# Performance work log

Measured on AMD Instinct MI355X. Metric: run time of the kernel, lower is better.

Reference implementation:

```python
import jax, jax.numpy as jnp
import numpy as np

NUM_SPECIES = 7
B, A, F = 1024, 48, 384


def setup_inputs() -> dict:
    key = jax.random.key(0)
    ks = jax.random.split(key, 10)
    species = jax.random.randint(ks[0], (B, A), 0, NUM_SPECIES, dtype=jnp.int32)
    aev = jax.random.normal(ks[1], (B, A, F), dtype=jnp.float32)
    def w(k, shape, fan_in):
        s = 1.0 / np.sqrt(fan_in).astype(np.float32)
        return jax.random.uniform(k, shape, jnp.float32, -s, s)
    return {
        "species": species,
        "aev": aev,
        "W1": w(ks[2], (NUM_SPECIES, 256, 384), 384),
        "b1": w(ks[3], (NUM_SPECIES, 256), 384),
        "W2": w(ks[4], (NUM_SPECIES, 192, 256), 256),
        "b2": w(ks[5], (NUM_SPECIES, 192), 256),
        "W3": w(ks[6], (NUM_SPECIES, 160, 192), 192),
        "b3": w(ks[7], (NUM_SPECIES, 160), 192),
        "W4": w(ks[8], (NUM_SPECIES, 1, 160), 160),
        "b4": w(ks[9], (NUM_SPECIES, 1), 160),
    }


def reference(species, aev, W1, b1, W2, b2, W3, b3, W4, b4):
    # species: [B, A] int, aev: [B, A, 384]
    celu = lambda x: jax.nn.celu(x, alpha=0.1)

    def expert(s):
        # Per-species MLP 384->256->192->160->1 applied to all atoms; selected via mask.
        h = celu(jnp.einsum('baf,hf->bah', aev, W1[s]) + b1[s])
        h = celu(jnp.einsum('bah,gh->bag', h, W2[s]) + b2[s])
        h = celu(jnp.einsum('bag,eg->bae', h, W3[s]) + b3[s])
        return (jnp.einsum('bae,oe->bao', h, W4[s]) + b4[s])[..., 0]  # [B, A]

    atom_energy = jnp.zeros(species.shape, aev.dtype)
    for s in range(NUM_SPECIES):  # fixed small expert loop (hard routing)
        atom_energy = jnp.where(species == s, expert(s), atom_energy)
    # scatter-sum atomic energies into per-molecule energies
    return atom_energy.sum(axis=1)  # [B]
```

## Files before the change

### kernel.cpp

```cpp
#include <hip/hip_runtime.h>
#include <math.h>

#define NSPEC 7
#define NMOL 1024
#define APM 48
#define NATOMS (NMOL * APM)
#define FDIM 384

typedef unsigned short u16;
typedef unsigned int u32;
typedef unsigned long long u64;
typedef __attribute__((ext_vector_type(8))) short short8;
typedef __attribute__((ext_vector_type(4))) float floatx4;

#define W1_ELEMS_PER_S (16 * 12 * 64 * 8)
#define W2_ELEMS_PER_S (12 * 8 * 64 * 8)
#define W3_ELEMS_PER_S (10 * 6 * 64 * 8)

#define BUCKET_BLOCKS (NATOMS / 256)
#define PACK1_BLOCKS (NSPEC * 16)
#define PACK2_BLOCKS (NSPEC * 12)
#define PACK3_BLOCKS (NSPEC * 10)
#define PREP_BLOCKS (BUCKET_BLOCKS + PACK1_BLOCKS + PACK2_BLOCKS + PACK3_BLOCKS)

#define MLP_BLOCKS 3078

#define WS_W1_OFF 32
#define WS_W2_OFF (WS_W1_OFF + 1376256)
#define WS_W3_OFF (WS_W2_OFF + 688128)
#define WS_BKT_OFF (WS_W3_OFF + 430080)

#define BUFST 264

__device__ __forceinline__ float celu01(float x) {
    float e = fmaf(0.1f, __expf(x * 10.0f), -0.1f);
    return x > 0.0f ? x : e;
}

__device__ __forceinline__ u16 bfr(float f) {
    u32 u = __float_as_uint(f);
    u += 0x7fffu + ((u >> 16) & 1u);
    return (u16)(u >> 16);
}

__device__ __forceinline__ float bf2f(short s) {
    return __uint_as_float(((u32)(u16)s) << 16);
}

union U8 { short8 v; u16 u[8]; };
union U4 { u64 ll; u16 u[4]; };

template <int KGS, int NTILES>
__device__ __forceinline__ void pack_tile(const float* __restrict__ W,
                                          u16* __restrict__ dst,
                                          int s, int t2, u16* lds) {
    const int K = KGS * 32;
    const int K4 = K / 4;
    int t = threadIdx.x;
    const float* wbase = W + ((size_t)(s * NTILES + t2) * 16) * K;
    for (int i = t; i < 16 * K4; i += 256) {
        int r = i / K4, c = i % K4;
        float4 v = ((const float4*)(wbase + (size_t)r * K))[c];
        u16* d = lds + r * K + c * 4;
        d[0] = bfr(v.x); d[1] = bfr(v.y); d[2] = bfr(v.z); d[3] = bfr(v.w);
    }
    __syncthreads();
    int w = t >> 6, lane = t & 63;
    int n = lane & 15, ks = lane >> 4;
    for (int kg = w; kg < KGS; kg += 4) {
        short8 v = *reinterpret_cast<const short8*>(lds + n * K + kg * 32 + ks * 8);
        *reinterpret_cast<short8*>(
            dst + (((size_t)(s * NTILES + t2) * KGS + kg) * 64 + lane) * 8) = v;
    }
}

__global__ void prep_kernel(const int* __restrict__ species,
                            int* __restrict__ g_cnt, u16* __restrict__ bucket,
                            const float* __restrict__ W1, const float* __restrict__ W2,
                            const float* __restrict__ W3,
                            u16* __restrict__ w1p, u16* __restrict__ w2p,
                            u16* __restrict__ w3p, float* __restrict__ out) {
    __shared__ u16 lds[16 * 384];
    __shared__ int l_cnt[NSPEC];
    __shared__ int l_base[NSPEC];
    int t = threadIdx.x;
    int bx = blockIdx.x;
    if (bx < BUCKET_BLOCKS) {
        if (bx == 0) {
            float4 z = {0.f, 0.f, 0.f, 0.f};
            ((float4*)out)[t] = z;
        }
        if (t < NSPEC) l_cnt[t] = 0;
        __syncthreads();
        int i = bx * 256 + t;
        int s = species[i];
        int lpos = atomicAdd(&l_cnt[s], 1);
        __syncthreads();
        if (t < NSPEC) l_base[t] = atomicAdd(&g_cnt[t], l_cnt[t]);
        __syncthreads();
        bucket[s * NATOMS + l_base[s] + lpos] = (u16)i;
    } else if (bx < BUCKET_BLOCKS + PACK1_BLOCKS) {
        int pid = bx - BUCKET_BLOCKS;
        pack_tile<12, 16>(W1, w1p, pid / 16, pid % 16, lds);
    } else if (bx < BUCKET_BLOCKS + PACK1_BLOCKS + PACK2_BLOCKS) {
        int pid = bx - (BUCKET_BLOCKS + PACK1_BLOCKS);
        pack_tile<8, 12>(W2, w2p, pid / 12, pid % 12, lds);
    } else {
        int pid = bx - (BUCKET_BLOCKS + PACK1_BLOCKS + PACK2_BLOCKS);
        pack_tile<6, 10>(W3, w3p, pid / 10, pid % 10, lds);
    }
}

template <int KGS, int NT, int DEPTH>
__device__ __forceinline__ void run_layer16(const short8* af,
                                            const u16* __restrict__ wsp,
                                            const float* __restrict__ bias,
                                            u16* __restrict__ outbuf, int lane) {
    const int HALF = KGS / 2;
    const int NH = NT * 2;
    const int nl = lane & 15, kg4 = lane >> 4;
    const u16* wb = wsp + (size_t)lane * 8;
    short8 b[DEPTH][HALF];
#pragma unroll
    for (int p = 0; p < DEPTH - 1; ++p)
#pragma unroll
        for (int k = 0; k < HALF; ++k)
            b[p][k] = *reinterpret_cast<const short8*>(wb + ((size_t)p * HALF + k) * 512);
    floatx4 acc = {0.f, 0.f, 0.f, 0.f};
#pragma unroll
    for (int h = 0; h < NH; ++h) {
        int pre = h + DEPTH - 1;
        if (pre < NH) {
#pragma unroll
            for (int k = 0; k < HALF; ++k)
                b[pre % DEPTH][k] = *reinterpret_cast<const short8*>(wb + ((size_t)pre * HALF + k) * 512);
        }
#pragma unroll
        for (int k = 0; k < HALF; ++k)
            acc = __builtin_amdgcn_mfma_f32_16x16x32_bf16(b[h % DEPTH][k], af[(h & 1) * HALF + k], acc, 0, 0, 0);
        if (h & 1) {
            int t = h >> 1;
            floatx4 bn = *reinterpret_cast<const floatx4*>(bias + t * 16 + kg4 * 4);
            U4 pk;
#pragma unroll
            for (int r = 0; r < 4; ++r)
                pk.u[r] = bfr(celu01(acc[r] + bn[r]));
            *reinterpret_cast<u64*>(outbuf + (size_t)nl * BUFST + t * 16 + kg4 * 4) = pk.ll;
            acc = (floatx4){0.f, 0.f, 0.f, 0.f};
        }
    }
}

template <int KGS>
__device__ __forceinline__ void load_a16(const u16* __restrict__ buf,
                                         short8* af, int lane) {
    int nl = lane & 15, kg4 = lane >> 4;
#pragma unroll
    for (int kg = 0; kg < KGS; ++kg)
        af[kg] = *reinterpret_cast<const short8*>(buf + (size_t)nl * BUFST + kg * 32 + kg4 * 8);
}

__global__ __launch_bounds__(64, 2) void mlp_kernel(
    const float* __restrict__ aev,
    const u16* __restrict__ w1p, const u16* __restrict__ w2p, const u16* __restrict__ w3p,
    const float* __restrict__ b1, const float* __restrict__ b2, const float* __restrict__ b3,
    const float* __restrict__ W4, const float* __restrict__ b4,
    const int* __restrict__ g_cnt, const u16* __restrict__ bucket,
    float* __restrict__ out) {
    int bx = blockIdx.x;
    int s = -1, chunk = 0;
    {
        int acc = 0;
#pragma unroll
        for (int q = 0; q < NSPEC; ++q) {
            int nb = (g_cnt[q] + 15) >> 4;
            if (s < 0 && bx < acc + nb) { s = q; chunk = bx - acc; }
            acc += nb;
        }
        if (s < 0) return;
    }
    int cnt = g_cnt[s];
    int lane = threadIdx.x & 63;
    int base = chunk * 16;

    __shared__ __align__(16) u16 buf[16 * BUFST];

    int nl = lane & 15, kg4 = lane >> 4;

    short8 af[12];
    {
        int i0 = base + nl;  if (i0 >= cnt) i0 = cnt - 1;
        int a0 = (int)bucket[s * NATOMS + i0];
        const float* ar0 = aev + (size_t)a0 * FDIM;
#pragma unroll
        for (int kg = 0; kg < 12; ++kg) {
            const float4* p0 = (const float4*)(ar0 + kg * 32 + kg4 * 8);
            float4 a = p0[0], b = p0[1];
            U8 x;
            x.u[0] = bfr(a.x); x.u[1] = bfr(a.y); x.u[2] = bfr(a.z); x.u[3] = bfr(a.w);
            x.u[4] = bfr(b.x); x.u[5] = bfr(b.y); x.u[6] = bfr(b.z); x.u[7] = bfr(b.w);
            af[kg] = x.v;
        }
    }
    run_layer16<12, 16, 4>(af, w1p + (size_t)s * W1_ELEMS_PER_S, b1 + s * 256, buf, lane);

    short8 c[8];
    load_a16<8>(buf, c, lane);
    run_layer16<8, 12, 4>(c, w2p + (size_t)s * W2_ELEMS_PER_S, b2 + s * 192, buf, lane);

    short8 d[6];
    load_a16<6>(buf, d, lane);
    run_layer16<6, 10, 4>(d, w3p + (size_t)s * W3_ELEMS_PER_S, b3 + s * 160, buf, lane);

    {
        int m = lane >> 2, q = lane & 3;
        const u16* h = buf + (size_t)m * BUFST + q * 40;
        const float* w4s = W4 + s * 160 + q * 40;
        float p = 0.f;
#pragma unroll
        for (int cc = 0; cc < 5; ++cc) {
            short8 hv = *reinterpret_cast<const short8*>(h + cc * 8);
            const float4* wp4 = (const float4*)(w4s + cc * 8);
            float4 wa = wp4[0], wb = wp4[1];
            p += bf2f(hv[0]) * wa.x + bf2f(hv[1]) * wa.y + bf2f(hv[2]) * wa.z + bf2f(hv[3]) * wa.w;
            p += bf2f(hv[4]) * wb.x + bf2f(hv[5]) * wb.y + bf2f(hv[6]) * wb.z + bf2f(hv[7]) * wb.w;
        }
        p += __shfl_down(p, 2, 4);
        p += __shfl_down(p, 1, 4);
        int idx = base + m;
        if (q == 0 && idx < cnt) {
            int atom = (int)bucket[s * NATOMS + idx];
            atomicAdd(&out[atom / APM], p + b4[s]);
        }
    }
}

extern "C" void kernel_launch(void* const* d_in, const int* in_sizes, int n_in,
                              void* d_out, int out_size, void* d_ws, size_t ws_size,
                              hipStream_t stream) {
    const int* species = (const int*)d_in[0];
    const float* aev = (const float*)d_in[1];
    const float* W1 = (const float*)d_in[2];
    const float* b1 = (const float*)d_in[3];
    const float* W2 = (const float*)d_in[4];
    const float* b2 = (const float*)d_in[5];
    const float* W3 = (const float*)d_in[6];
    const float* b3 = (const float*)d_in[7];
    const float* W4 = (const float*)d_in[8];
    const float* b4 = (const float*)d_in[9];
    float* out = (float*)d_out;

    unsigned char* wsb = (unsigned char*)d_ws;
    int* g_cnt = (int*)wsb;
    u16* w1p = (u16*)(wsb + WS_W1_OFF);
    u16* w2p = (u16*)(wsb + WS_W2_OFF);
    u16* w3p = (u16*)(wsb + WS_W3_OFF);
    u16* bucket = (u16*)(wsb + WS_BKT_OFF);

    hipMemsetAsync(g_cnt, 0, 8 * sizeof(int), stream);

    prep_kernel<<<PREP_BLOCKS, 256, 0, stream>>>(
        species, g_cnt, bucket, W1, W2, W3, w1p, w2p, w3p, out);

    mlp_kernel<<<MLP_BLOCKS, 64, 0, stream>>>(
        aev, w1p, w2p, w3p, b1, b2, b3, W4, b4, g_cnt, bucket, out);
}
```

Measured before the change: 180.2 us.

## Share packed weight tiles across four waves via double-buffered LDS staging

Measured after the change: 187.0 us. +3.8%, slower.

```diff
diff --git a/kernel.cpp b/kernel.cpp
--- a/kernel.cpp
+++ b/kernel.cpp
@@ -23,7 +23,7 @@
 #define PACK3_BLOCKS (NSPEC * 10)
 #define PREP_BLOCKS (BUCKET_BLOCKS + PACK1_BLOCKS + PACK2_BLOCKS + PACK3_BLOCKS)
 
-#define MLP_BLOCKS 3078
+#define MLP_BLOCKS 774
 
 #define WS_W1_OFF 32
 #define WS_W2_OFF (WS_W1_OFF + 1376256)
@@ -31,6 +31,12 @@
 #define WS_BKT_OFF (WS_W3_OFF + 430080)
 
 #define BUFST 264
+#define SLOT_U16 6144
+
+#define GLD_LDS(gsrc, ldst)                                                   \
+    __builtin_amdgcn_global_load_lds(                                         \
+        (const __attribute__((address_space(1))) unsigned int*)(gsrc),        \
+        (__attribute__((address_space(3))) unsigned int*)(ldst), 16, 0, 0)
 
 __device__ __forceinline__ float celu01(float x) {
     float e = fmaf(0.1f, __expf(x * 10.0f), -0.1f);
@@ -111,43 +117,42 @@
     }
 }
 
-template <int KGS, int NT, int DEPTH>
-__device__ __forceinline__ void run_layer16(const short8* af,
-                                            const u16* __restrict__ wsp,
-                                            const float* __restrict__ bias,
-                                            u16* __restrict__ outbuf, int lane) {
-    const int HALF = KGS / 2;
-    const int NH = NT * 2;
+template <int KGS, int NT, int SWEEPS>
+__device__ __forceinline__ void run_layer_staged(
+    const short8* af, const u16* __restrict__ wsp,
+    const float* __restrict__ bias,
+    u16* __restrict__ outbuf,
+    u16* __restrict__ sb, int lane, int w) {
     const int nl = lane & 15, kg4 = lane >> 4;
-    const u16* wb = wsp + (size_t)lane * 8;
-    short8 b[DEPTH][HALF];
-#pragma unroll
-    for (int p = 0; p < DEPTH - 1; ++p)
-#pragma unroll
-        for (int k = 0; k < HALF; ++k)
-            b[p][k] = *reinterpret_cast<const short8*>(wb + ((size_t)p * HALF + k) * 512);
-    floatx4 acc = {0.f, 0.f, 0.f, 0.f};
-#pragma unroll
-    for (int h = 0; h < NH; ++h) {
-        int pre = h + DEPTH - 1;
-        if (pre < NH) {
-#pragma unroll
-            for (int k = 0; k < HALF; ++k)
-                b[pre % DEPTH][k] = *reinterpret_cast<const short8*>(wb + ((size_t)pre * HALF + k) * 512);
-        }
-#pragma unroll
-        for (int k = 0; k < HALF; ++k)
-            acc = __builtin_amdgcn_mfma_f32_16x16x32_bf16(b[h % DEPTH][k], af[(h & 1) * HALF + k], acc, 0, 0, 0);
-        if (h & 1) {
-            int t = h >> 1;
-            floatx4 bn = *reinterpret_cast<const floatx4*>(bias + t * 16 + kg4 * 4);
-            U4 pk;
-#pragma unroll
-            for (int r = 0; r < 4; ++r)
-                pk.u[r] = bfr(celu01(acc[r] + bn[r]));
-            *reinterpret_cast<u64*>(outbuf + (size_t)nl * BUFST + t * 16 + kg4 * 4) = pk.ll;
-            acc = (floatx4){0.f, 0.f, 0.f, 0.f};
-        }
+#pragma unroll
+    for (int sw = 0; sw < SWEEPS; ++sw)
+        GLD_LDS(wsp + sw * 2048 + w * 512 + lane * 8, sb + sw * 2048 + w * 512);
+#pragma unroll 1
+    for (int t = 0; t < NT; ++t) {
+        u16* cur = sb + (t & 1) * SLOT_U16;
+        u16* nxt = sb + ((t & 1) ^ 1) * SLOT_U16;
+        __syncthreads();
+        if (t + 1 < NT) {
+            const u16* tn = wsp + (size_t)(t + 1) * KGS * 512;
+#pragma unroll
+            for (int sw = 0; sw < SWEEPS; ++sw)
+                GLD_LDS(tn + sw * 2048 + w * 512 + lane * 8, nxt + sw * 2048 + w * 512);
+        }
+        __syncthreads();
+        short8 bb[KGS];
+#pragma unroll
+        for (int kg = 0; kg < KGS; ++kg)
+            bb[kg] = *reinterpret_cast<const short8*>(cur + kg * 512 + lane * 8);
+        floatx4 acc = {0.f, 0.f, 0.f, 0.f};
+#pragma unroll
+        for (int kg = 0; kg < KGS; ++kg)
+            acc = __builtin_amdgcn_mfma_f32_16x16x32_bf16(bb[kg], af[kg], acc, 0, 0, 0);
+        floatx4 bn = *reinterpret_cast<const floatx4*>(bias + t * 16 + kg4 * 4);
+        U4 pk;
+#pragma unroll
+        for (int r = 0; r < 4; ++r)
+            pk.u[r] = bfr(celu01(acc[r] + bn[r]));
+        *reinterpret_cast<u64*>(outbuf + (size_t)nl * BUFST + t * 16 + kg4 * 4) = pk.ll;
     }
 }
 
@@ -160,7 +165,7 @@
         af[kg] = *reinterpret_cast<const short8*>(buf + (size_t)nl * BUFST + kg * 32 + kg4 * 8);
 }
 
-__global__ __launch_bounds__(64, 2) void mlp_kernel(
+__global__ __launch_bounds__(256, 2) void mlp_kernel(
     const float* __restrict__ aev,
     const u16* __restrict__ w1p, const u16* __restrict__ w2p, const u16* __restrict__ w3p,
     const float* __restrict__ b1, const float* __restrict__ b2, const float* __restrict__ b3,
@@ -173,23 +178,25 @@
         int acc = 0;
 #pragma unroll
         for (int q = 0; q < NSPEC; ++q) {
-            int nb = (g_cnt[q] + 15) >> 4;
+            int nb = (g_cnt[q] + 63) >> 6;
             if (s < 0 && bx < acc + nb) { s = q; chunk = bx - acc; }
             acc += nb;
         }
         if (s < 0) return;
     }
     int cnt = g_cnt[s];
-    int lane = threadIdx.x & 63;
-    int base = chunk * 16;
-
-    __shared__ __align__(16) u16 buf[16 * BUFST];
+    int w = threadIdx.x >> 6, lane = threadIdx.x & 63;
+    int wbase = chunk * 64 + w * 16;
+
+    __shared__ __align__(16) u16 act[4][16 * BUFST];
+    __shared__ __align__(16) u16 sb[2 * SLOT_U16];
+    u16* buf = &act[w][0];
 
     int nl = lane & 15, kg4 = lane >> 4;
 
     short8 af[12];
     {
-        int i0 = base + nl;  if (i0 >= cnt) i0 = cnt - 1;
+        int i0 = wbase + nl;  if (i0 >= cnt) i0 = cnt > 0 ? cnt - 1 : 0;
         int a0 = (int)bucket[s * NATOMS + i0];
         const float* ar0 = aev + (size_t)a0 * FDIM;
 #pragma unroll
@@ -202,15 +209,18 @@
             af[kg] = x.v;
         }
     }
-    run_layer16<12, 16, 4>(af, w1p + (size_t)s * W1_ELEMS_PER_S, b1 + s * 256, buf, lane);
+    run_layer_staged<12, 16, 3>(af, w1p + (size_t)s * W1_ELEMS_PER_S, b1 + s * 256,
+                                buf, sb, lane, w);
 
     short8 c[8];
     load_a16<8>(buf, c, lane);
-    run_layer16<8, 12, 4>(c, w2p + (size_t)s * W2_ELEMS_PER_S, b2 + s * 192, buf, lane);
+    run_layer_staged<8, 12, 2>(c, w2p + (size_t)s * W2_ELEMS_PER_S, b2 + s * 192,
+                               buf, sb, lane, w);
 
     short8 d[6];
     load_a16<6>(buf, d, lane);
-    run_layer16<6, 10, 4>(d, w3p + (size_t)s * W3_ELEMS_PER_S, b3 + s * 160, buf, lane);
+    run_layer_staged<6, 10, 2>(d, w3p + (size_t)s * W3_ELEMS_PER_S, b3 + s * 160,
+                               buf, sb, lane, w);
 
     {
         int m = lane >> 2, q = lane & 3;
@@ -227,7 +237,7 @@
         }
         p += __shfl_down(p, 2, 4);
         p += __shfl_down(p, 1, 4);
-        int idx = base + m;
+        int idx = wbase + m;
         if (q == 0 && idx < cnt) {
             int atom = (int)bucket[s * NATOMS + idx];
             atomicAdd(&out[atom / APM], p + b4[s]);
@@ -262,6 +272,6 @@
     prep_kernel<<<PREP_BLOCKS, 256, 0, stream>>>(
         species, g_cnt, bucket, W1, W2, W3, w1p, w2p, w3p, out);
 
-    mlp_kernel<<<MLP_BLOCKS, 64, 0, stream>>>(
+    mlp_kernel<<<MLP_BLOCKS, 256, 0, stream>>>(
         aev, w1p, w2p, w3p, b1, b2, b3, W4, b4, g_cnt, bucket, out);
 }
```
